# Kernel optimization log

Hardware: AMD Instinct MI355X
Metric: run time of the kernel (lower is better)

Reference implementation:

```python
import jax, jax.numpy as jnp
import numpy as np
from jax import lax

B, T, IDIM, HDIM = 128, 256, 64, 128
TS, KS, OC1, ANF = 64, 3, 100, 64
S1 = TS - 3 * (KS - 1)   # 58: three VALID ks=3 stride-1 convs
S = S1 * S1              # 3364
HN = 2 * HDIM            # 256 = h_dim * l_dim (l_dim=2)
F = S + HN               # 3620
HID = F // 2             # 1810


def _conv(x, w, b):
    y = lax.conv_general_dilated(x, w, (1, 1), 'VALID',
                                 dimension_numbers=('NCHW', 'OIHW', 'NCHW'))
    return y + b[None, :, None, None]


def _lstm_layer(x, w_ih, w_hh, b_ih, b_hh):
    # x: [B, T, D] -> (outputs [B, T, H], final hidden [B, H]); PyTorch gate order i,f,g,o
    Bn = x.shape[0]
    h0 = jnp.zeros((Bn, HDIM), x.dtype)
    c0 = jnp.zeros((Bn, HDIM), x.dtype)
    def step(carry, xt):
        h, c = carry
        g = xt @ w_ih.T + h @ w_hh.T + b_ih + b_hh
        i, f, gg, o = jnp.split(g, 4, axis=-1)
        c = jax.nn.sigmoid(f) * c + jax.nn.sigmoid(i) * jnp.tanh(gg)
        h = jax.nn.sigmoid(o) * jnp.tanh(c)
        return (h, c), h
    (hT, cT), ys = lax.scan(step, (h0, c0), jnp.swapaxes(x, 0, 1))
    return jnp.swapaxes(ys, 0, 1), hT


def setup_inputs() -> dict:
    key = jax.random.key(0)
    k = jax.random.split(key, 30)
    s = 0.05
    H4 = 4 * HDIM
    return {
        'x1': jax.random.normal(k[0], (B, 3, TS, TS), jnp.float32),
        'x2': jax.random.normal(k[1], (B, T, IDIM), jnp.float32),
        # conv2a/conv2b: two Monte-Carlo weight samples of the same Bayesian conv2 layer
        'conv1_w': jax.random.normal(k[2], (OC1, 3, KS, KS), jnp.float32) * s,
        'conv1_b': jax.random.normal(k[3], (OC1,), jnp.float32) * s,
        'conv2a_w': jax.random.normal(k[4], (OC1, OC1, KS, KS), jnp.float32) * s,
        'conv2a_b': jax.random.normal(k[5], (OC1,), jnp.float32) * s,
        'conv2b_w': jax.random.normal(k[6], (OC1, OC1, KS, KS), jnp.float32) * s,
        'conv2b_b': jax.random.normal(k[7], (OC1,), jnp.float32) * s,
        'w_ih0': jax.random.normal(k[8], (H4, IDIM), jnp.float32) * s,
        'w_hh0': jax.random.normal(k[9], (H4, HDIM), jnp.float32) * s,
        'b_ih0': jax.random.normal(k[10], (H4,), jnp.float32) * s,
        'b_hh0': jax.random.normal(k[11], (H4,), jnp.float32) * s,
        'w_ih1': jax.random.normal(k[12], (H4, HDIM), jnp.float32) * s,
        'w_hh1': jax.random.normal(k[13], (H4, HDIM), jnp.float32) * s,
        'b_ih1': jax.random.normal(k[14], (H4,), jnp.float32) * s,
        'b_hh1': jax.random.normal(k[15], (H4,), jnp.float32) * s,
        'attn1_w': jax.random.normal(k[16], (ANF, F), jnp.float32) * s,
        'attn1_b': jax.random.normal(k[17], (ANF,), jnp.float32) * s,
        'attn2_w': jax.random.normal(k[18], (1, ANF), jnp.float32) * s,
        'attn2_b': jax.random.normal(k[19], (1,), jnp.float32) * s,
        'fc1_w': jax.random.normal(k[20], (HID, F), jnp.float32) * s,
        'fc1_b': jax.random.normal(k[21], (HID,), jnp.float32) * s,
        'fc2_w': jax.random.normal(k[22], (1, HID), jnp.float32) * s,
        'fc2_b': jax.random.normal(k[23], (1,), jnp.float32) * s,
    }


def reference(x1, x2, conv1_w, conv1_b, conv2a_w, conv2a_b, conv2b_w, conv2b_b,
              w_ih0, w_hh0, b_ih0, b_hh0, w_ih1, w_hh1, b_ih1, b_hh1,
              attn1_w, attn1_b, attn2_w, attn2_b, fc1_w, fc1_b, fc2_w, fc2_b):
    Bn = x1.shape[0]
    # CNN branch
    x = jax.nn.relu(_conv(x1, conv1_w, conv1_b))
    x = jax.nn.relu(_conv(x, conv2a_w, conv2a_b))
    x = jax.nn.relu(_conv(x, conv2b_w, conv2b_b))
    xd = x.reshape(Bn, OC1, S)                               # [B, oc1, S]
    # LSTM branch (2 layers, dropout in eval mode = identity)
    y0, h0f = _lstm_layer(x2, w_ih0, w_hh0, b_ih0, b_hh0)
    _, h1f = _lstm_layer(y0, w_ih1, w_hh1, b_ih1, b_hh1)
    hn = jnp.concatenate([h0f, h1f], axis=1)                 # [B, 2*h_dim]
    # Broadcast hidden state across channels (replaces the torch concat loop)
    hn_b = jnp.broadcast_to(hn[:, None, :], (Bn, OC1, HN))
    fused = jnp.concatenate([xd, hn_b], axis=2)              # [B, oc1, F]
    # Attention
    a = jnp.tanh(fused @ attn1_w.T + attn1_b)                # [B, oc1, anf]
    a = a @ attn2_w.T + attn2_b                              # [B, oc1, 1]
    a = jax.nn.softmax(a, axis=1)
    ctx = jnp.einsum('bcs,bco->bso', xd, a).reshape(Bn, S)   # [B, S]
    # Fusion MLP (dropout eval-mode identity)
    m = jnp.concatenate([ctx, hn], axis=1)                   # [B, F]
    h = jax.nn.relu(m @ fc1_w.T + fc1_b)
    return h @ fc2_w.T + fc2_b                               # [B, 1]
```

## Files before the change

kernel.cpp:

```cpp
#include <hip/hip_runtime.h>
#include <hip/hip_bf16.h>
#include <math.h>

#define BB 128
#define TT 256
#define IDIM 64
#define HD 128
#define G4 512
#define OC 100
#define W1 62
#define W2 60
#define W3 58
#define NPX1 (W1*W1)
#define NPX2 (W2*W2)
#define NPX3 (W3*W3)
#define SS NPX3
#define FF (SS + 2*HD)
#define HIDN 1810
#define ANF 64

typedef __hip_bfloat16 bf16;
typedef _Float16 f16;
typedef __attribute__((ext_vector_type(8))) short bf16x8;
typedef __attribute__((ext_vector_type(4))) short bf16x4;
typedef __attribute__((ext_vector_type(2))) _Float16 half2v;
typedef __attribute__((ext_vector_type(4))) float f32x4;

__device__ __forceinline__ float ldf(const float* p) { return *p; }
__device__ __forceinline__ float ldf(const bf16* p)  { return __bfloat162float(*p); }
__device__ __forceinline__ void  stf(float* p, float v) { *p = v; }
__device__ __forceinline__ void  stf(bf16* p, float v)  { *p = __float2bfloat16(v); }

__device__ __forceinline__ short f2bs(float v) {
    bf16 t = __float2bfloat16(v); short s; __builtin_memcpy(&s, &t, 2); return s;
}
__device__ __forceinline__ float fsig(float x) {
    return __builtin_amdgcn_rcpf(1.f + __expf(-x));
}
__device__ __forceinline__ float ftanh(float x) {
    float t = __expf(-2.f * fabsf(x));
    float r = __builtin_amdgcn_rcpf(1.f + t);
    float m = 1.f - 2.f * t * r;
    return copysignf(m, x);
}
__device__ __forceinline__ float fmix2(unsigned w, unsigned h, float acc) {
    half2v wv, hv;
    __builtin_memcpy(&wv, &w, 4);
    __builtin_memcpy(&hv, &h, 4);
    acc = fmaf((float)wv[0], (float)hv[0], acc);
    acc = fmaf((float)wv[1], (float)hv[1], acc);
    return acc;
}

__device__ __forceinline__ bf16x8 load8(const bf16* p) { return *(const bf16x8*)p; }
__device__ __forceinline__ bf16x8 load8(const float* p) {
    float4 x = *(const float4*)p;
    float4 y = *(const float4*)(p + 4);
    bf16x8 r;
    r[0] = f2bs(x.x); r[1] = f2bs(x.y); r[2] = f2bs(x.z); r[3] = f2bs(x.w);
    r[4] = f2bs(y.x); r[5] = f2bs(y.y); r[6] = f2bs(y.z); r[7] = f2bs(y.w);
    return r;
}

__global__ void zero_kernel(float* o, int n)
{
    int i = blockIdx.x * 256 + threadIdx.x;
    if (i < n) o[i] = 0.f;
}

__device__ __forceinline__ void body_cvt_bf16(const float* __restrict__ s, bf16* __restrict__ d,
                                              int i, int n4)
{
    if (i >= n4) return;
    float4 v = ((const float4*)s)[i];
    bf16x4 o;
    o[0] = f2bs(v.x); o[1] = f2bs(v.y); o[2] = f2bs(v.z); o[3] = f2bs(v.w);
    *(bf16x4*)(d + 4 * (size_t)i) = o;
}
__device__ __forceinline__ void body_cvt_f16(const float* __restrict__ s, f16* __restrict__ d,
                                             int i, int n4)
{
    if (i >= n4) return;
    float4 v = ((const float4*)s)[i];
    f16 o[4] = {(f16)v.x, (f16)v.y, (f16)v.z, (f16)v.w};
    *(uint2*)(d + 4 * (size_t)i) = *(uint2*)o;
}
__device__ __forceinline__ void body_wt(const float* __restrict__ w, bf16* __restrict__ WT, int idx)
{
    if (idx >= 129024) return;
    int i  = idx & 31;
    int oc = (idx >> 5) % 112;
    int ts = idx / (112 * 32);
    int s = ts & 3, t = ts >> 2;
    int ic = s * 32 + i;
    float v = 0.f;
    if (oc < OC && ic < OC) v = w[(oc * OC + ic) * 9 + t];
    WT[idx] = __float2bfloat16(v);
}

__global__ __launch_bounds__(256)
void prep_kernel(const float* __restrict__ x2,   bf16* __restrict__ X2B,
                 const float* __restrict__ whh0, f16*  __restrict__ LWf0,
                 const float* __restrict__ whh1, f16*  __restrict__ LWf1,
                 const float* __restrict__ wih0, bf16* __restrict__ WIH0B,
                 const float* __restrict__ wih1, bf16* __restrict__ WIH1B,
                 const float* __restrict__ a1w,  bf16* __restrict__ A1WB,
                 const float* __restrict__ bih0, const float* __restrict__ bhh0, float* __restrict__ BS0,
                 const float* __restrict__ bih1, const float* __restrict__ bhh1, float* __restrict__ BS1,
                 const float* __restrict__ c2aw, bf16* __restrict__ WTa,
                 const float* __restrict__ c2bw, bf16* __restrict__ WTb)
{
    int bid = blockIdx.x;
    int tid = threadIdx.x;
    if (bid < 2048)      body_cvt_bf16(x2,   X2B,   bid * 256 + tid, 524288);
    else if (bid < 2112) body_cvt_f16 (whh0, LWf0, (bid - 2048) * 256 + tid, 16384);
    else if (bid < 2176) body_cvt_f16 (whh1, LWf1, (bid - 2112) * 256 + tid, 16384);
    else if (bid < 2208) body_cvt_bf16(wih0, WIH0B, (bid - 2176) * 256 + tid, 8192);
    else if (bid < 2272) body_cvt_bf16(wih1, WIH1B, (bid - 2208) * 256 + tid, 16384);
    else if (bid < 2499) body_cvt_bf16(a1w,  A1WB,  (bid - 2272) * 256 + tid, 57920);
    else if (bid < 2500) { BS0[tid] = bih0[tid] + bhh0[tid]; BS0[tid + 256] = bih0[tid + 256] + bhh0[tid + 256]; }
    else if (bid < 2501) { BS1[tid] = bih1[tid] + bhh1[tid]; BS1[tid + 256] = bih1[tid + 256] + bhh1[tid + 256]; }
    else if (bid < 3005) body_wt(c2aw, WTa, (bid - 2501) * 256 + tid);
    else                 body_wt(c2bw, WTb, (bid - 3005) * 256 + tid);
}

__global__ __launch_bounds__(256)
void conv1_kernel(const float* __restrict__ x1,
                  const float* __restrict__ w,
                  const float* __restrict__ bias,
                  bf16* __restrict__ out)
{
    __shared__ float wl[2700];
    __shared__ float bl[OC];
    int tid = threadIdx.x;
    for (int i = tid; i < 2700; i += 256) wl[i] = w[i];
    if (tid < OC) bl[tid] = bias[tid];
    __syncthreads();
    int b  = blockIdx.x;
    int px = blockIdx.y * 256 + tid;
    if (px >= NPX1) return;
    int y = px / W1, x = px % W1;
    float in[3][3][3];
    const float* xb = x1 + (size_t)b * 3 * 64 * 64;
#pragma unroll
    for (int ic = 0; ic < 3; ic++)
#pragma unroll
        for (int r = 0; r < 3; r++)
#pragma unroll
            for (int c = 0; c < 3; c++)
                in[ic][r][c] = xb[(ic * 64 + y + r) * 64 + x + c];
    bf16* ob = out + (size_t)b * OC * NPX1 + px;
    for (int oc = 0; oc < OC; ++oc) {
        float acc = bl[oc];
        const float* wp = &wl[oc * 27];
#pragma unroll
        for (int ic = 0; ic < 3; ic++)
#pragma unroll
            for (int r = 0; r < 3; r++)
#pragma unroll
                for (int c = 0; c < 3; c++)
                    acc = fmaf(in[ic][r][c], wp[ic * 9 + r * 3 + c], acc);
        ob[(size_t)oc * NPX1] = __float2bfloat16(fmaxf(acc, 0.f));
    }
}

__global__ __launch_bounds__(512, 1)
void conv2_mfma(const bf16* __restrict__ in,
                const bf16* __restrict__ WT,
                const float* __restrict__ bias,
                bf16* __restrict__ out,
                int iw, int ow)
{
    __shared__ bf16 il[10 * 72 * 40];
    __shared__ bf16 wl[4032 * 8];
    int tid = threadIdx.x;
    int b = blockIdx.x;
    int y0 = blockIdx.y * 8;
    int wid = tid >> 6;
    int l = tid & 63;
    int hq = l >> 4;
    int l16 = l & 15;
    int yo = y0 + wid;

    f32x4 acc[7][4];
#pragma unroll
    for (int f = 0; f < 7; f++) {
#pragma unroll
        for (int r = 0; r < 4; r++) {
            int oc = f * 16 + hq * 4 + r;
            float bv = (oc < OC) ? bias[oc] : 0.f;
#pragma unroll
            for (int n = 0; n < 4; n++) acc[f][n][r] = bv;
        }
    }

    const size_t ims = (size_t)iw * iw;
    int icl = tid & 31;
    int t2  = tid >> 5;
    for (int s = 0; s < 4; ++s) {
        __syncthreads();
        int ic = s * 32 + icl;
        bool icok = ic < OC;
        const bf16* ibase = in + (size_t)(b * OC + ic) * ims;
#pragma unroll
        for (int it = 0; it < 6; ++it) {
            int u2 = t2 + it * 16;
            if (u2 < 90) {
                int r = u2 / 9, xb = u2 - r * 9;
                int x8 = xb * 8;
                int yy = y0 + r;
                bf16x8 v = {0, 0, 0, 0, 0, 0, 0, 0};
                if (icok && yy < iw && x8 < iw) {
                    const short* sp = (const short*)(ibase + (size_t)yy * iw + x8);
                    if (x8 + 8 <= iw) {
                        const unsigned* sp32 = (const unsigned*)sp;
#pragma unroll
                        for (int q = 0; q < 4; q++)
                            ((unsigned*)&v)[q] = sp32[q];
                    } else {
                        for (int k = 0; k < 8; k++)
                            if (x8 + k < iw) ((short*)&v)[k] = sp[k];
                    }
                }
                bf16* dst = &il[(r * 72 + x8) * 40 + icl];
#pragma unroll
                for (int k = 0; k < 8; k++)
                    *(short*)&dst[k * 40] = ((short*)&v)[k];
            }
        }
#pragma unroll
        for (int it = 0; it < 8; ++it) {
            int u = tid + it * 512;
            if (u < 4032) {
                int tf = u >> 6; int lp = u & 63;
                int t = tf / 7, f = tf - t * 7;
                int oc = f * 16 + (lp & 15);
                int hq2 = lp >> 4;
                *(bf16x8*)&wl[(size_t)u * 8] =
                    *(const bf16x8*)(WT + (size_t)((t * 4 + s) * 112 + oc) * 32 + hq2 * 8);
            }
        }
        __syncthreads();

#pragma unroll
        for (int ky = 0; ky < 3; ++ky) {
#pragma unroll
            for (int kx = 0; kx < 3; ++kx) {
                int t = ky * 3 + kx;
                bf16x8 a[7];
#pragma unroll
                for (int f = 0; f < 7; f++)
                    a[f] = *(const bf16x8*)&wl[(size_t)((t * 7 + f) * 64 + l) * 8];
                bf16x8 bfr[4];
#pragma unroll
                for (int n = 0; n < 4; n++)
                    bfr[n] = *(const bf16x8*)&il[((wid + ky) * 72 + kx + l16 + n * 16) * 40 + hq * 8];
#pragma unroll
                for (int f = 0; f < 7; f++)
#pragma unroll
                    for (int n = 0; n < 4; n++)
                        acc[f][n] = __builtin_amdgcn_mfma_f32_16x16x32_bf16(
                            a[f], bfr[n], acc[f][n], 0, 0, 0);
            }
        }
    }

    if (yo < ow) {
#pragma unroll
        for (int f = 0; f < 7; f++) {
#pragma unroll
            for (int r = 0; r < 4; r++) {
                int oc = f * 16 + hq * 4 + r;
                if (oc < OC) {
#pragma unroll
                    for (int n = 0; n < 4; n++) {
                        int x = n * 16 + l16;
                        if (x < ow)
                            out[((size_t)(b * OC + oc) * ow + yo) * ow + x] =
                                __float2bfloat16(fmaxf(acc[f][n][r], 0.f));
                    }
                }
            }
        }
    }
}

template<typename TB, typename TC, int ACT>
__global__ __launch_bounds__(256)
void gemm_mfma(const bf16* __restrict__ A, int lda,
               const TB* __restrict__ B, int ldb,
               const float* __restrict__ bias,
               TC* __restrict__ C, int ldc,
               int M, int N, int K)
{
    __shared__ bf16 As[64 * 72];
    __shared__ bf16 Bs[64 * 72];
    int tid = threadIdx.x;
    int l = tid & 63, wid = tid >> 6;
    int l16 = l & 15, h = l >> 4;
    int m0 = blockIdx.x * 64, n0 = blockIdx.y * 64;
    f32x4 acc[4];
#pragma unroll
    for (int nb = 0; nb < 4; nb++) acc[nb] = (f32x4){0.f, 0.f, 0.f, 0.f};

    int rs = tid >> 3;
    int kc = (tid & 7) * 8;

    for (int k0 = 0; k0 < K; k0 += 64) {
        int kr = K - k0;
#pragma unroll
        for (int half = 0; half < 2; half++) {
            int rr = rs + half * 32;
            bf16x8 av = {0, 0, 0, 0, 0, 0, 0, 0};
            int m = m0 + rr;
            if (m < M) {
                const short* src = (const short*)(A + (size_t)m * lda + k0 + kc);
                if (kc + 8 <= kr) av = *(const bf16x8*)src;
                else if (kc < kr) {
                    for (int j = 0; j < 8; j++) if (kc + j < kr) ((short*)&av)[j] = src[j];
                }
            }
            *(bf16x8*)&As[rr * 72 + kc] = av;
            bf16x8 bv = {0, 0, 0, 0, 0, 0, 0, 0};
            int n = n0 + rr;
            if (n < N) {
                const TB* src = B + (size_t)n * ldb + k0 + kc;
                if (kc + 8 <= kr) bv = load8(src);
                else if (kc < kr) {
                    for (int j = 0; j < 8; j++) if (kc + j < kr) ((short*)&bv)[j] = f2bs(ldf(src + j));
                }
            }
            *(bf16x8*)&Bs[rr * 72 + kc] = bv;
        }
        __syncthreads();
#pragma unroll
        for (int kk = 0; kk < 2; kk++) {
            bf16x8 af = *(const bf16x8*)&As[(wid * 16 + l16) * 72 + kk * 32 + h * 8];
#pragma unroll
            for (int nb = 0; nb < 4; nb++) {
                bf16x8 bfr = *(const bf16x8*)&Bs[(nb * 16 + l16) * 72 + kk * 32 + h * 8];
                acc[nb] = __builtin_amdgcn_mfma_f32_16x16x32_bf16(af, bfr, acc[nb], 0, 0, 0);
            }
        }
        __syncthreads();
    }
#pragma unroll
    for (int nb = 0; nb < 4; nb++) {
        int col = n0 + nb * 16 + l16;
        if (col >= N) continue;
        float bv = bias ? bias[col] : 0.f;
#pragma unroll
        for (int reg = 0; reg < 4; reg++) {
            int row = m0 + wid * 16 + h * 4 + reg;
            if (row < M) {
                float v = acc[nb][reg] + bv;
                if (ACT == 1) v = fmaxf(v, 0.f);
                stf(&C[(size_t)row * ldc + col], v);
            }
        }
    }
}

template<typename TA, typename TC, int BM, int BN, int BK, int TM, int TN, int ACT>
__global__ __launch_bounds__((BM / TM) * (BN / TN))
void gemm_tn(const TA* __restrict__ A, int lda,
             const float* __restrict__ Bmat, int ldb,
             const float* __restrict__ bias,
             TC* __restrict__ C, int ldc,
             int M, int N, int K)
{
    constexpr int TX = BN / TN;
    constexpr int TY = BM / TM;
    constexpr int NT = TX * TY;
    __shared__ float As[BK][BM + 1];
    __shared__ float Bs[BK][BN + 1];
    int tid = threadIdx.x;
    int tx = tid % TX, ty = tid / TX;
    int m0 = blockIdx.x * BM, n0 = blockIdx.y * BN;
    float acc[TM][TN] = {};
    for (int k0 = 0; k0 < K; k0 += BK) {
        for (int idx = tid; idx < BM * BK; idx += NT) {
            int i = idx / BK, j = idx % BK;
            int m = m0 + i, k = k0 + j;
            As[j][i] = (m < M && k < K) ? ldf(&A[(size_t)m * lda + k]) : 0.f;
        }
        for (int idx = tid; idx < BN * BK; idx += NT) {
            int i = idx / BK, j = idx % BK;
            int n = n0 + i, k = k0 + j;
            Bs[j][i] = (n < N && k < K) ? Bmat[(size_t)n * ldb + k] : 0.f;
        }
        __syncthreads();
#pragma unroll
        for (int k = 0; k < BK; ++k) {
            float av[TM], bv[TN];
#pragma unroll
            for (int i = 0; i < TM; i++) av[i] = As[k][ty * TM + i];
#pragma unroll
            for (int j = 0; j < TN; j++) bv[j] = Bs[k][tx * TN + j];
#pragma unroll
            for (int i = 0; i < TM; i++)
#pragma unroll
                for (int j = 0; j < TN; j++)
                    acc[i][j] += av[i] * bv[j];
        }
        __syncthreads();
    }
#pragma unroll
    for (int i = 0; i < TM; i++) {
        int m = m0 + ty * TM + i;
        if (m >= M) continue;
#pragma unroll
        for (int j = 0; j < TN; j++) {
            int n = n0 + tx * TN + j;
            if (n >= N) continue;
            float v = acc[i][j] + (bias ? bias[n] : 0.f);
            if (ACT == 1) v = fmaxf(v, 0.f);
            stf(&C[(size_t)m * ldc + n], v);
        }
    }
}

__global__ __launch_bounds__(512, 1)
void lstm_recur(const bf16* __restrict__ G,
                const f16* __restrict__ LWr,
                bf16* __restrict__ Y,
                float* __restrict__ HN,
                int hoff)
{
    __shared__ __align__(16) f16 hl[HD];
    __shared__ float ex[G4];
    int g = threadIdx.x;
    int b = blockIdx.x;
    uint4 wv[16];
    const uint4* wp = (const uint4*)(LWr + (size_t)g * HD);
#pragma unroll
    for (int q = 0; q < 16; q++) wv[q] = wp[q];
#pragma unroll
    for (int q = 0; q < 16; q++)
        asm volatile("" : "+v"(wv[q].x), "+v"(wv[q].y), "+v"(wv[q].z), "+v"(wv[q].w));
    float c = 0.f;
    if (g < HD) hl[g] = (f16)0.f;
    __syncthreads();
    const bf16* Gb = G + (size_t)b * TT * G4 + g;
    float gcur = __bfloat162float(Gb[0]);
    for (int t = 0; t < TT; ++t) {
        int tn = (t + 1 < TT) ? t + 1 : t;
        bf16 gnext = Gb[(size_t)tn * G4];
        float a0 = 0.f, a1 = 0.f, a2 = 0.f, a3 = 0.f;
#pragma unroll
        for (int q = 0; q < 16; q++) {
            uint4 hw = *(const uint4*)&hl[q * 8];
            a0 = fmix2(wv[q].x, hw.x, a0);
            a1 = fmix2(wv[q].y, hw.y, a1);
            a2 = fmix2(wv[q].z, hw.z, a2);
            a3 = fmix2(wv[q].w, hw.w, a3);
        }
        float dot = gcur + (a0 + a1) + (a2 + a3);
        float tr;
        if (g < 2 * HD || g >= 3 * HD) tr = fsig(dot);
        else tr = ftanh(dot);
        ex[g] = tr;
        gcur = __bfloat162float(gnext);
        __syncthreads();
        if (g < HD) {
            float iv = ex[g], fv = ex[HD + g], gv = ex[2 * HD + g], ov = ex[3 * HD + g];
            c = fv * c + iv * gv;
            float nh = ov * ftanh(c);
            hl[g] = (f16)nh;
            if (Y) Y[((size_t)b * TT + t) * HD + g] = __float2bfloat16(nh);
            if (t == TT - 1) HN[(size_t)b * 256 + hoff + g] = nh;
        }
        __syncthreads();
    }
}

__global__ __launch_bounds__(128)
void attn_softmax(const float* __restrict__ T1,
                  const float* __restrict__ HB,
                  const float* __restrict__ a2w,
                  const float* __restrict__ a2b,
                  float* __restrict__ ATT)
{
    __shared__ float hbl[ANF];
    __shared__ float awl[ANF];
    __shared__ float red[128];
    int b = blockIdx.x, tid = threadIdx.x;
    if (tid < ANF) { hbl[tid] = HB[b * ANF + tid]; awl[tid] = a2w[tid]; }
    __syncthreads();
    float lg = -1e30f;
    if (tid < OC) {
        const float* tp = T1 + (size_t)(b * OC + tid) * ANF;
        float s = 0.f;
#pragma unroll 4
        for (int j = 0; j < ANF; j++) s += ftanh(tp[j] + hbl[j]) * awl[j];
        lg = s + a2b[0];
    }
    red[tid] = lg; __syncthreads();
    for (int st = 64; st > 0; st >>= 1) { if (tid < st) red[tid] = fmaxf(red[tid], red[tid + st]); __syncthreads(); }
    float mx = red[0]; __syncthreads();
    float e = (tid < OC) ? __expf(lg - mx) : 0.f;
    red[tid] = e; __syncthreads();
    for (int st = 64; st > 0; st >>= 1) { if (tid < st) red[tid] += red[tid + st]; __syncthreads(); }
    if (tid < OC) ATT[b * OC + tid] = e / red[0];
}

__global__ __launch_bounds__(256)
void ctx_concat(const bf16* __restrict__ XD,
                const float* __restrict__ ATT,
                const float* __restrict__ HN,
                bf16* __restrict__ M)
{
    __shared__ float al[OC];
    int b = blockIdx.x;
    int tid = threadIdx.x;
    if (tid < OC) al[tid] = ATT[b * OC + tid];
    __syncthreads();
    int s = blockIdx.y * 256 + tid;
    if (s < SS) {
        const bf16* xp = XD + (size_t)b * OC * SS + s;
        float acc = 0.f;
#pragma unroll 4
        for (int c = 0; c < OC; c++) acc = fmaf(__bfloat162float(xp[(size_t)c * SS]), al[c], acc);
        M[(size_t)b * FF + s] = __float2bfloat16(acc);
    } else if (s < FF) {
        M[(size_t)b * FF + s] = __float2bfloat16(HN[b * 256 + (s - SS)]);
    }
}

__global__ __launch_bounds__(256)
void fc2_kernel(const float* __restrict__ H1,
                const float* __restrict__ w,
                const float* __restrict__ bias,
                float* __restrict__ out)
{
    int tid = threadIdx.x;
    int lane = tid & 63, wid = tid >> 6;
    int b = blockIdx.x * 4 + wid;
    float acc = 0.f;
    for (int j = lane; j < HIDN; j += 64) acc = fmaf(H1[(size_t)b * HIDN + j], w[j], acc);
#pragma unroll
    for (int off = 32; off > 0; off >>= 1) acc += __shfl_down(acc, off, 64);
    if (lane == 0) out[b] = acc + bias[0];
}

extern "C" void kernel_launch(void* const* d_in, const int* in_sizes, int n_in,
                              void* d_out, int out_size, void* d_ws, size_t ws_size,
                              hipStream_t stream)
{
    const float* x1   = (const float*)d_in[0];
    const float* x2   = (const float*)d_in[1];
    const float* c1w  = (const float*)d_in[2];
    const float* c1b  = (const float*)d_in[3];
    const float* c2aw = (const float*)d_in[4];
    const float* c2ab = (const float*)d_in[5];
    const float* c2bw = (const float*)d_in[6];
    const float* c2bb = (const float*)d_in[7];
    const float* wih0 = (const float*)d_in[8];
    const float* whh0 = (const float*)d_in[9];
    const float* bih0 = (const float*)d_in[10];
    const float* bhh0 = (const float*)d_in[11];
    const float* wih1 = (const float*)d_in[12];
    const float* whh1 = (const float*)d_in[13];
    const float* bih1 = (const float*)d_in[14];
    const float* bhh1 = (const float*)d_in[15];
    const float* a1w  = (const float*)d_in[16];
    const float* a1b  = (const float*)d_in[17];
    const float* a2w  = (const float*)d_in[18];
    const float* a2b  = (const float*)d_in[19];
    const float* f1w  = (const float*)d_in[20];
    const float* f1b  = (const float*)d_in[21];
    const float* f2w  = (const float*)d_in[22];
    const float* f2b  = (const float*)d_in[23];
    float* out = (float*)d_out;

    char* base = (char*)d_ws;
    bf16* G0    = (bf16*)(base + 0);
    bf16* Y0    = (bf16*)(base + 33554432);
    bf16* G1    = G0;
    bf16* X2B   = (bf16*)(base + 41943040);
    bf16* WIH0B = (bf16*)(base + 46137344);
    bf16* WIH1B = (bf16*)(base + 46202880);
    f16*  LWf0  = (f16*)(base + 46333952);
    f16*  LWf1  = (f16*)(base + 46465024);
    const size_t LSTM_END = 46596096;

    int nb = 0; size_t ov = 0;
    for (int cand = BB; cand >= 32; cand >>= 1) {
        size_t cnn = (size_t)cand * OC * (NPX1 + NPX2) * 2;
        size_t o = cnn > LSTM_END ? cnn : LSTM_END;
        size_t q = o + 2048 + 2048 + 131072 + 32768
                 + (size_t)cand * OC * 64 * 4
                 + (((size_t)cand * OC * 4 + 255) & ~(size_t)255)
                 + 926720 + 926720 + 258048 + 258048 + 463360;
        if (ws_size >= q) { nb = cand; ov = o; break; }
    }
    if (nb == 0) {
        zero_kernel<<<1, 128, 0, stream>>>(out, out_size);
        return;
    }
    bf16* A1c = (bf16*)(base + 0);
    bf16* A2c = (bf16*)(base + (size_t)nb * OC * NPX1 * 2);
    bf16* XDc = A1c;
    size_t p = ov;
    float* BS0  = (float*)(base + p); p += 2048;
    float* BS1  = (float*)(base + p); p += 2048;
    float* HN   = (float*)(base + p); p += 131072;
    float* HB   = (float*)(base + p); p += 32768;
    float* T1c  = (float*)(base + p); p += (size_t)nb * OC * 64 * 4;
    float* ATTc = (float*)(base + p); p += ((size_t)nb * OC * 4 + 255) & ~(size_t)255;
    bf16*  MBb  = (bf16*)(base + p); p += 926720;
    float* H1   = (float*)(base + p); p += 926720;
    bf16* WTa   = (bf16*)(base + p); p += 258048;
    bf16* WTb   = (bf16*)(base + p); p += 258048;
    bf16* A1WB  = (bf16*)(base + p); p += 463360;

    prep_kernel<<<3509, 256, 0, stream>>>(
        x2, X2B, whh0, LWf0, whh1, LWf1, wih0, WIH0B, wih1, WIH1B, a1w, A1WB,
        bih0, bhh0, BS0, bih1, bhh1, BS1, c2aw, WTa, c2bw, WTb);

    gemm_mfma<bf16, bf16, 0><<<dim3(512, 8), 256, 0, stream>>>(
        X2B, IDIM, WIH0B, IDIM, BS0, G0, G4, BB * TT, G4, IDIM);
    lstm_recur<<<BB, 512, 0, stream>>>(G0, LWf0, Y0, HN, 0);
    gemm_mfma<bf16, bf16, 0><<<dim3(512, 8), 256, 0, stream>>>(
        Y0, HD, WIH1B, HD, BS1, G1, G4, BB * TT, G4, HD);
    lstm_recur<<<BB, 512, 0, stream>>>(G1, LWf1, (bf16*)nullptr, HN, HD);

    gemm_tn<float, float, 32, 32, 16, 2, 2, 0><<<dim3(4, 2), 256, 0, stream>>>(
        HN, 256, a1w + SS, FF, a1b, HB, ANF, BB, ANF, 256);

    for (int c0 = 0; c0 < BB; c0 += nb) {
        conv1_kernel<<<dim3(nb, 16), 256, 0, stream>>>(
            x1 + (size_t)c0 * 3 * 64 * 64, c1w, c1b, A1c);
        conv2_mfma<<<dim3(nb, 8), 512, 0, stream>>>(A1c, WTa, c2ab, A2c, W1, W2);
        conv2_mfma<<<dim3(nb, 8), 512, 0, stream>>>(A2c, WTb, c2bb, XDc, W2, W3);
        gemm_mfma<bf16, float, 0><<<dim3(nb * OC / 64, 1), 256, 0, stream>>>(
            XDc, SS, A1WB, FF, nullptr, T1c, ANF, nb * OC, ANF, SS);
        attn_softmax<<<nb, 128, 0, stream>>>(T1c, HB + (size_t)c0 * ANF, a2w, a2b, ATTc);
        ctx_concat<<<dim3(nb, 15), 256, 0, stream>>>(
            XDc, ATTc, HN + (size_t)c0 * 256, MBb + (size_t)c0 * FF);
    }

    gemm_mfma<float, float, 1><<<dim3(2, 29), 256, 0, stream>>>(
        MBb, FF, f1w, FF, f1b, H1, HIDN, BB, HIDN, FF);
    fc2_kernel<<<BB / 4, 256, 0, stream>>>(H1, f2w, f2b, out);
}
```

Baseline: 1.192 ms.

## Co-schedule layer-0 LSTM recurrence with conv1 in one hybrid kernel launch

Adds a hybrid kernel whose first 128 blocks run the layer-0 LSTM recurrence while the remaining blocks compute conv1. The latency-bound recurrence uses only 128 CUs, so conv1 can fill the idle CUs. When the whole batch fits in workspace, the launch sequence is reordered and the A1/A2 buffers are swapped so conv1's output does not overlap the LSTM buffers. The chunked path is kept as a fallback. Risk: conv1 blocks could delay LSTM block scheduling, and conv1 now runs 512-thread blocks under launch_bounds(512,1).

```diff
diff --git a/kernel.cpp b/kernel.cpp
--- a/kernel.cpp
+++ b/kernel.cpp
@@ -124,11 +124,40 @@
     else                 body_wt(c2bw, WTb, (bid - 3005) * 256 + tid);
 }
 
+__device__ __forceinline__
+void conv1_body(const float* __restrict__ x1, const float* __restrict__ wl,
+                const float* __restrict__ bl, bf16* __restrict__ out, int b, int py, int t)
+{
+    int px = py * 256 + t;
+    if (px >= NPX1) return;
+    int y = px / W1, x = px % W1;
+    float in[3][3][3];
+    const float* xb = x1 + (size_t)b * 3 * 64 * 64;
+#pragma unroll
+    for (int ic = 0; ic < 3; ic++)
+#pragma unroll
+        for (int r = 0; r < 3; r++)
+#pragma unroll
+            for (int c = 0; c < 3; c++)
+                in[ic][r][c] = xb[(ic * 64 + y + r) * 64 + x + c];
+    bf16* ob = out + (size_t)b * OC * NPX1 + px;
+    for (int oc = 0; oc < OC; ++oc) {
+        float acc = bl[oc];
+        const float* wp = &wl[oc * 27];
+#pragma unroll
+        for (int ic = 0; ic < 3; ic++)
+#pragma unroll
+            for (int r = 0; r < 3; r++)
+#pragma unroll
+                for (int c = 0; c < 3; c++)
+                    acc = fmaf(in[ic][r][c], wp[ic * 9 + r * 3 + c], acc);
+        ob[(size_t)oc * NPX1] = __float2bfloat16(fmaxf(acc, 0.f));
+    }
+}
+
 __global__ __launch_bounds__(256)
-void conv1_kernel(const float* __restrict__ x1,
-                  const float* __restrict__ w,
-                  const float* __restrict__ bias,
-                  bf16* __restrict__ out)
+void conv1_kernel(const float* __restrict__ x1, const float* __restrict__ w,
+                  const float* __restrict__ bias, bf16* __restrict__ out)
 {
     __shared__ float wl[2700];
     __shared__ float bl[OC];
@@ -136,46 +165,16 @@
     for (int i = tid; i < 2700; i += 256) wl[i] = w[i];
     if (tid < OC) bl[tid] = bias[tid];
     __syncthreads();
-    int b  = blockIdx.x;
-    int px = blockIdx.y * 256 + tid;
-    if (px >= NPX1) return;
-    int y = px / W1, x = px % W1;
-    float in[3][3][3];
-    const float* xb = x1 + (size_t)b * 3 * 64 * 64;
-#pragma unroll
-    for (int ic = 0; ic < 3; ic++)
-#pragma unroll
-        for (int r = 0; r < 3; r++)
-#pragma unroll
-            for (int c = 0; c < 3; c++)
-                in[ic][r][c] = xb[(ic * 64 + y + r) * 64 + x + c];
-    bf16* ob = out + (size_t)b * OC * NPX1 + px;
-    for (int oc = 0; oc < OC; ++oc) {
-        float acc = bl[oc];
-        const float* wp = &wl[oc * 27];
-#pragma unroll
-        for (int ic = 0; ic < 3; ic++)
-#pragma unroll
-            for (int r = 0; r < 3; r++)
-#pragma unroll
-                for (int c = 0; c < 3; c++)
-                    acc = fmaf(in[ic][r][c], wp[ic * 9 + r * 3 + c], acc);
-        ob[(size_t)oc * NPX1] = __float2bfloat16(fmaxf(acc, 0.f));
-    }
-}
-
-__global__ __launch_bounds__(512, 1)
-void conv2_mfma(const bf16* __restrict__ in,
-                const bf16* __restrict__ WT,
-                const float* __restrict__ bias,
-                bf16* __restrict__ out,
-                int iw, int ow)
-{
-    __shared__ bf16 il[10 * 72 * 40];
-    __shared__ bf16 wl[4032 * 8];
-    int tid = threadIdx.x;
-    int b = blockIdx.x;
-    int y0 = blockIdx.y * 8;
+    conv1_body(x1, wl, bl, out, blockIdx.x, blockIdx.y, tid);
+}
+
+__device__ __forceinline__
+void conv2_body(const bf16* __restrict__ in, const bf16* __restrict__ WT,
+                const float* __restrict__ bias, bf16* __restrict__ out,
+                int iw, int ow, int b, int yblk, int tid,
+                bf16* __restrict__ il, bf16* __restrict__ wl)
+{
+    int y0 = yblk * 8;
     int wid = tid >> 6;
     int l = tid & 63;
     int hq = l >> 4;
@@ -282,6 +281,96 @@
                 }
             }
         }
+    }
+}
+
+__global__ __launch_bounds__(512, 1)
+void conv2_mfma(const bf16* __restrict__ in, const bf16* __restrict__ WT,
+                const float* __restrict__ bias, bf16* __restrict__ out,
+                int iw, int ow)
+{
+    __shared__ bf16 il[10 * 72 * 40];
+    __shared__ bf16 wl[4032 * 8];
+    conv2_body(in, WT, bias, out, iw, ow, blockIdx.x, blockIdx.y, threadIdx.x, il, wl);
+}
+
+__device__ __forceinline__
+void lstm_body(const bf16* __restrict__ G, const f16* __restrict__ LWr,
+               bf16* __restrict__ Y, float* __restrict__ HN, int hoff,
+               int b, int g, f16* __restrict__ hl, float* __restrict__ ex)
+{
+    uint4 wv[16];
+    const uint4* wp = (const uint4*)(LWr + (size_t)g * HD);
+#pragma unroll
+    for (int q = 0; q < 16; q++) wv[q] = wp[q];
+#pragma unroll
+    for (int q = 0; q < 16; q++)
+        asm volatile("" : "+v"(wv[q].x), "+v"(wv[q].y), "+v"(wv[q].z), "+v"(wv[q].w));
+    float c = 0.f;
+    if (g < HD) hl[g] = (f16)0.f;
+    __syncthreads();
+    const bf16* Gb = G + (size_t)b * TT * G4 + g;
+    float gcur = __bfloat162float(Gb[0]);
+    for (int t = 0; t < TT; ++t) {
+        int tn = (t + 1 < TT) ? t + 1 : t;
+        bf16 gnext = Gb[(size_t)tn * G4];
+        float a0 = 0.f, a1 = 0.f, a2 = 0.f, a3 = 0.f;
+#pragma unroll
+        for (int q = 0; q < 16; q++) {
+            uint4 hw = *(const uint4*)&hl[q * 8];
+            a0 = fmix2(wv[q].x, hw.x, a0);
+            a1 = fmix2(wv[q].y, hw.y, a1);
+            a2 = fmix2(wv[q].z, hw.z, a2);
+            a3 = fmix2(wv[q].w, hw.w, a3);
+        }
+        float dot = gcur + (a0 + a1) + (a2 + a3);
+        float tr;
+        if (g < 2 * HD || g >= 3 * HD) tr = fsig(dot);
+        else tr = ftanh(dot);
+        ex[g] = tr;
+        gcur = __bfloat162float(gnext);
+        __syncthreads();
+        if (g < HD) {
+            float iv = ex[g], fv = ex[HD + g], gv = ex[2 * HD + g], ov = ex[3 * HD + g];
+            c = fv * c + iv * gv;
+            float nh = ov * ftanh(c);
+            hl[g] = (f16)nh;
+            if (Y) Y[((size_t)b * TT + t) * HD + g] = __float2bfloat16(nh);
+            if (t == TT - 1) HN[(size_t)b * 256 + hoff + g] = nh;
+        }
+        __syncthreads();
+    }
+}
+
+__global__ __launch_bounds__(512, 1)
+void lstm_recur(const bf16* __restrict__ G, const f16* __restrict__ LWr,
+                bf16* __restrict__ Y, float* __restrict__ HN, int hoff)
+{
+    __shared__ __align__(16) f16 hl[HD];
+    __shared__ float ex[G4];
+    lstm_body(G, LWr, Y, HN, hoff, blockIdx.x, threadIdx.x, hl, ex);
+}
+
+__global__ __launch_bounds__(512, 1)
+void hybrid_l0c1(const bf16* __restrict__ G, const f16* __restrict__ LWf0,
+                 bf16* __restrict__ Y0, float* __restrict__ HN,
+                 const float* __restrict__ x1, const float* __restrict__ c1w,
+                 const float* __restrict__ c1b, bf16* __restrict__ A1)
+{
+    __shared__ __align__(16) char smem[11264];
+    int bid = blockIdx.x;
+    if (bid < BB) {
+        lstm_body(G, LWf0, Y0, HN, 0, bid, threadIdx.x,
+                  (f16*)smem, (float*)(smem + 512));
+    } else {
+        float* wl = (float*)smem;
+        float* bl = (float*)(smem + 10800);
+        int tid = threadIdx.x;
+        for (int i = tid; i < 2700; i += 512) wl[i] = c1w[i];
+        if (tid < OC) bl[tid] = c1b[tid];
+        __syncthreads();
+        int v = (bid - BB) * 2 + (tid >> 8);
+        conv1_body(x1, wl, bl, A1, v >> 4, v & 15, tid & 255);
     }
 }
 
@@ -420,60 +509,6 @@
     }
 }
 
-__global__ __launch_bounds__(512, 1)
-void lstm_recur(const bf16* __restrict__ G,
-                const f16* __restrict__ LWr,
-                bf16* __restrict__ Y,
-                float* __restrict__ HN,
-                int hoff)
-{
-    __shared__ __align__(16) f16 hl[HD];
-    __shared__ float ex[G4];
-    int g = threadIdx.x;
-    int b = blockIdx.x;
-    uint4 wv[16];
-    const uint4* wp = (const uint4*)(LWr + (size_t)g * HD);
-#pragma unroll
-    for (int q = 0; q < 16; q++) wv[q] = wp[q];
-#pragma unroll
-    for (int q = 0; q < 16; q++)
-        asm volatile("" : "+v"(wv[q].x), "+v"(wv[q].y), "+v"(wv[q].z), "+v"(wv[q].w));
-    float c = 0.f;
-    if (g < HD) hl[g] = (f16)0.f;
-    __syncthreads();
-    const bf16* Gb = G + (size_t)b * TT * G4 + g;
-    float gcur = __bfloat162float(Gb[0]);
-    for (int t = 0; t < TT; ++t) {
-        int tn = (t + 1 < TT) ? t + 1 : t;
-        bf16 gnext = Gb[(size_t)tn * G4];
-        float a0 = 0.f, a1 = 0.f, a2 = 0.f, a3 = 0.f;
-#pragma unroll
-        for (int q = 0; q < 16; q++) {
-            uint4 hw = *(const uint4*)&hl[q * 8];
-            a0 = fmix2(wv[q].x, hw.x, a0);
-            a1 = fmix2(wv[q].y, hw.y, a1);
-            a2 = fmix2(wv[q].z, hw.z, a2);
-            a3 = fmix2(wv[q].w, hw.w, a3);
-        }
-        float dot = gcur + (a0 + a1) + (a2 + a3);
-        float tr;
-        if (g < 2 * HD || g >= 3 * HD) tr = fsig(dot);
-        else tr = ftanh(dot);
-        ex[g] = tr;
-        gcur = __bfloat162float(gnext);
-        __syncthreads();
-        if (g < HD) {
-            float iv = ex[g], fv = ex[HD + g], gv = ex[2 * HD + g], ov = ex[3 * HD + g];
-            c = fv * c + iv * gv;
-            float nh = ov * ftanh(c);
-            hl[g] = (f16)nh;
-            if (Y) Y[((size_t)b * TT + t) * HD + g] = __float2bfloat16(nh);
-            if (t == TT - 1) HN[(size_t)b * 256 + hoff + g] = nh;
-        }
-        __syncthreads();
-    }
-}
-
 __global__ __launch_bounds__(128)
 void attn_softmax(const float* __restrict__ T1,
                   const float* __restrict__ HB,
@@ -528,10 +563,8 @@
 }
 
 __global__ __launch_bounds__(256)
-void fc2_kernel(const float* __restrict__ H1,
-                const float* __restrict__ w,
-                const float* __restrict__ bias,
-                float* __restrict__ out)
+void fc2_kernel(const float* __restrict__ H1, const float* __restrict__ w,
+                const float* __restrict__ bias, float* __restrict__ out)
 {
     int tid = threadIdx.x;
     int lane = tid & 63, wid = tid >> 6;
@@ -598,8 +631,15 @@
         zero_kernel<<<1, 128, 0, stream>>>(out, out_size);
         return;
     }
-    bf16* A1c = (bf16*)(base + 0);
-    bf16* A2c = (bf16*)(base + (size_t)nb * OC * NPX1 * 2);
+    bf16* A1c;
+    bf16* A2c;
+    if (nb == BB) {
+        A2c = (bf16*)(base + 0);
+        A1c = (bf16*)(base + (size_t)BB * OC * NPX2 * 2);
+    } else {
+        A1c = (bf16*)(base + 0);
+        A2c = (bf16*)(base + (size_t)nb * OC * NPX1 * 2);
+    }
     bf16* XDc = A1c;
     size_t p = ov;
     float* BS0  = (float*)(base + p); p += 2048;
@@ -620,24 +660,39 @@
 
     gemm_mfma<bf16, bf16, 0><<<dim3(512, 8), 256, 0, stream>>>(
         X2B, IDIM, WIH0B, IDIM, BS0, G0, G4, BB * TT, G4, IDIM);
-    lstm_recur<<<BB, 512, 0, stream>>>(G0, LWf0, Y0, HN, 0);
-    gemm_mfma<bf16, bf16, 0><<<dim3(512, 8), 256, 0, stream>>>(
-        Y0, HD, WIH1B, HD, BS1, G1, G4, BB * TT, G4, HD);
-    lstm_recur<<<BB, 512, 0, stream>>>(G1, LWf1, (bf16*)nullptr, HN, HD);
-
-    gemm_tn<float, float, 32, 32, 16, 2, 2, 0><<<dim3(4, 2), 256, 0, stream>>>(
-        HN, 256, a1w + SS, FF, a1b, HB, ANF, BB, ANF, 256);
-
-    for (int c0 = 0; c0 < BB; c0 += nb) {
-        conv1_kernel<<<dim3(nb, 16), 256, 0, stream>>>(
-            x1 + (size_t)c0 * 3 * 64 * 64, c1w, c1b, A1c);
-        conv2_mfma<<<dim3(nb, 8), 512, 0, stream>>>(A1c, WTa, c2ab, A2c, W1, W2);
-        conv2_mfma<<<dim3(nb, 8), 512, 0, stream>>>(A2c, WTb, c2bb, XDc, W2, W3);
-        gemm_mfma<bf16, float, 0><<<dim3(nb * OC / 64, 1), 256, 0, stream>>>(
-            XDc, SS, A1WB, FF, nullptr, T1c, ANF, nb * OC, ANF, SS);
-        attn_softmax<<<nb, 128, 0, stream>>>(T1c, HB + (size_t)c0 * ANF, a2w, a2b, ATTc);
-        ctx_concat<<<dim3(nb, 15), 256, 0, stream>>>(
-            XDc, ATTc, HN + (size_t)c0 * 256, MBb + (size_t)c0 * FF);
+
+    if (nb == BB) {
+        hybrid_l0c1<<<BB + BB * 8, 512, 0, stream>>>(
+            G0, LWf0, Y0, HN, x1, c1w, c1b, A1c);
+        gemm_mfma<bf16, bf16, 0><<<dim3(512, 8), 256, 0, stream>>>(
+            Y0, HD, WIH1B, HD, BS1, G1, G4, BB * TT, G4, HD);
+        lstm_recur<<<BB, 512, 0, stream>>>(G1, LWf1, (bf16*)nullptr, HN, HD);
+        conv2_mfma<<<dim3(BB, 8), 512, 0, stream>>>(A1c, WTa, c2ab, A2c, W1, W2);
+        conv2_mfma<<<dim3(BB, 8), 512, 0, stream>>>(A2c, WTb, c2bb, XDc, W2, W3);
+        gemm_tn<float, float, 32, 32, 16, 2, 2, 0><<<dim3(4, 2), 256, 0, stream>>>(
+            HN, 256, a1w + SS, FF, a1b, HB, ANF, BB, ANF, 256);
+        gemm_mfma<bf16, float, 0><<<dim3(BB * OC / 64, 1), 256, 0, stream>>>(
+            XDc, SS, A1WB, FF, nullptr, T1c, ANF, BB * OC, ANF, SS);
+        attn_softmax<<<BB, 128, 0, stream>>>(T1c, HB, a2w, a2b, ATTc);
+        ctx_concat<<<dim3(BB, 15), 256, 0, stream>>>(XDc, ATTc, HN, MBb);
+    } else {
+        lstm_recur<<<BB, 512, 0, stream>>>(G0, LWf0, Y0, HN, 0);
+        gemm_mfma<bf16, bf16, 0><<<dim3(512, 8), 256, 0, stream>>>(
+            Y0, HD, WIH1B, HD, BS1, G1, G4, BB * TT, G4, HD);
+        lstm_recur<<<BB, 512, 0, stream>>>(G1, LWf1, (bf16*)nullptr, HN, HD);
+        gemm_tn<float, float, 32, 32, 16, 2, 2, 0><<<dim3(4, 2), 256, 0, stream>>>(
+            HN, 256, a1w + SS, FF, a1b, HB, ANF, BB, ANF, 256);
+        for (int c0 = 0; c0 < BB; c0 += nb) {
+            conv1_kernel<<<dim3(nb, 16), 256, 0, stream>>>(
+                x1 + (size_t)c0 * 3 * 64 * 64, c1w, c1b, A1c);
+            conv2_mfma<<<dim3(nb, 8), 512, 0, stream>>>(A1c, WTa, c2ab, A2c, W1, W2);
+            conv2_mfma<<<dim3(nb, 8), 512, 0, stream>>>(A2c, WTb, c2bb, XDc, W2, W3);
+            gemm_mfma<bf16, float, 0><<<dim3(nb * OC / 64, 1), 256, 0, stream>>>(
+                XDc, SS, A1WB, FF, nullptr, T1c, ANF, nb * OC, ANF, SS);
+            attn_softmax<<<nb, 128, 0, stream>>>(T1c, HB + (size_t)c0 * ANF, a2w, a2b, ATTc);
+            ctx_concat<<<dim3(nb, 15), 256, 0, stream>>>(
+                XDc, ATTc, HN + (size_t)c0 * 256, MBb + (size_t)c0 * FF);
+        }
     }
 
     gemm_mfma<float, float, 1><<<dim3(2, 29), 256, 0, stream>>>(
```

New measurement: 1.098 ms. -7.8%, faster.
